# Optimization experiments

Measured on AMD Instinct MI355X. Metric: run time of the kernel, lower is better.

Reference implementation:

```python
import jax, jax.numpy as jnp
import numpy as np

HID = 10


def _lstm_cell(xt, h, c, W_ih, W_hh, b_ih, b_hh):
    # PyTorch LSTMCell: gates ordered (i, f, g, o)
    gates = xt @ W_ih.T + b_ih + h @ W_hh.T + b_hh  # [B, 4*HID]
    i, f, g, o = jnp.split(gates, 4, axis=-1)
    c_new = jax.nn.sigmoid(f) * c + jax.nn.sigmoid(i) * jnp.tanh(g)
    h_new = jax.nn.sigmoid(o) * jnp.tanh(c_new)
    return h_new, c_new


def setup_inputs() -> dict:
    key = jax.random.key(0)
    ks = jax.random.split(key, 12)
    B, T = 2048, 1024
    s = 0.1
    return {
        "x": jax.random.normal(ks[0], (B, T), dtype=jnp.float32),
        "W_ih1": jax.random.normal(ks[1], (4 * HID, 1), dtype=jnp.float32) * s,
        "W_hh1": jax.random.normal(ks[2], (4 * HID, HID), dtype=jnp.float32) * s,
        "b_ih1": jax.random.normal(ks[3], (4 * HID,), dtype=jnp.float32) * s,
        "b_hh1": jax.random.normal(ks[4], (4 * HID,), dtype=jnp.float32) * s,
        "W_ih2": jax.random.normal(ks[5], (4 * HID, HID), dtype=jnp.float32) * s,
        "W_hh2": jax.random.normal(ks[6], (4 * HID, HID), dtype=jnp.float32) * s,
        "b_ih2": jax.random.normal(ks[7], (4 * HID,), dtype=jnp.float32) * s,
        "b_ih2b": None,  # placeholder removed below
        "b_hh2": jax.random.normal(ks[8], (4 * HID,), dtype=jnp.float32) * s,
        "W_lin": jax.random.normal(ks[9], (1, HID), dtype=jnp.float32) * s,
        "b_lin": jax.random.normal(ks[10], (1,), dtype=jnp.float32) * s,
        "future": 64,
    } if False else {
        "x": jax.random.normal(ks[0], (B, T), dtype=jnp.float32),
        "W_ih1": jax.random.normal(ks[1], (4 * HID, 1), dtype=jnp.float32) * s,
        "W_hh1": jax.random.normal(ks[2], (4 * HID, HID), dtype=jnp.float32) * s,
        "b_ih1": jax.random.normal(ks[3], (4 * HID,), dtype=jnp.float32) * s,
        "b_hh1": jax.random.normal(ks[4], (4 * HID,), dtype=jnp.float32) * s,
        "W_ih2": jax.random.normal(ks[5], (4 * HID, HID), dtype=jnp.float32) * s,
        "W_hh2": jax.random.normal(ks[6], (4 * HID, HID), dtype=jnp.float32) * s,
        "b_ih2": jax.random.normal(ks[7], (4 * HID,), dtype=jnp.float32) * s,
        "b_hh2": jax.random.normal(ks[8], (4 * HID,), dtype=jnp.float32) * s,
        "W_lin": jax.random.normal(ks[9], (1, HID), dtype=jnp.float32) * s,
        "b_lin": jax.random.normal(ks[10], (1,), dtype=jnp.float32) * s,
        "future": 64,
    }


def _forward(x, W_ih1, W_hh1, b_ih1, b_hh1, W_ih2, W_hh2, b_ih2, b_hh2,
             W_lin, b_lin, future):
    B = x.shape[0]
    z = jnp.zeros((B, HID), dtype=x.dtype)
    state0 = (z, z, z, z)  # h1, c1, h2, c2

    def step(state, xt):
        h1, c1, h2, c2 = state
        h1, c1 = _lstm_cell(xt, h1, c1, W_ih1, W_hh1, b_ih1, b_hh1)
        h2, c2 = _lstm_cell(h1, h2, c2, W_ih2, W_hh2, b_ih2, b_hh2)
        y = h2 @ W_lin.T + b_lin  # [B, 1]
        return (h1, c1, h2, c2), y

    xs = x.T[:, :, None]  # [T, B, 1]
    state, ys = jax.lax.scan(step, state0, xs)  # ys: [T, B, 1]
    outs = ys[:, :, 0].T  # [B, T]

    if future > 0:
        last = ys[-1]  # [B, 1]

        def fstep(carry, _):
            state, y = carry
            state, y_new = step(state, y)
            return (state, y_new), y_new

        (_, _), fys = jax.lax.scan(fstep, (state, last), None, length=future)
        outs = jnp.concatenate([outs, fys[:, :, 0].T], axis=1)
    return outs  # [B, T + future]


def reference(x, W_ih1, W_hh1, b_ih1, b_hh1, W_ih2, W_hh2, b_ih2, b_hh2,
              W_lin, b_lin, future):
    return _forward(x, W_ih1, W_hh1, b_ih1, b_hh1, W_ih2, W_hh2, b_ih2,
                    b_hh2, W_lin, b_lin, future)
```

## Files before the change

kernel.cpp:

```cpp
#include <hip/hip_runtime.h>


#define NB 512
#define TMAIN 1024
#define HID 10
#define KCH 16
#define NCH (TMAIN / KCH)

typedef float v2f __attribute__((ext_vector_type(2)));
typedef float v4f __attribute__((ext_vector_type(4)));

#define PIN2(v) asm volatile("" : "+v"(v))
#define PIN(v)  asm volatile("" : "+v"(v))

__device__ __forceinline__ float rcp_(float v)  { return __builtin_amdgcn_rcpf(v); }
__device__ __forceinline__ float exp2_(float v) { return __builtin_amdgcn_exp2f(v); }
__device__ __forceinline__ v2f mk2(float x, float y) { v2f r; r.x = x; r.y = y; return r; }
__device__ __forceinline__ v2f pfma2(v2f a, v2f b, v2f c) { return __builtin_elementwise_fma(a, b, c); }

template<int J>
__device__ __forceinline__ float bc16(float v) {
    return __int_as_float(__builtin_amdgcn_ds_swizzle(__float_as_int(v), (J << 5) | 0x10));
}
__device__ __forceinline__ void bcast10(float h, float* hb) {
    hb[0] = bc16<0>(h); hb[1] = bc16<1>(h); hb[2] = bc16<2>(h); hb[3] = bc16<3>(h);
    hb[4] = bc16<4>(h); hb[5] = bc16<5>(h); hb[6] = bc16<6>(h); hb[7] = bc16<7>(h);
    hb[8] = bc16<8>(h); hb[9] = bc16<9>(h);
}

__global__ __launch_bounds__(128)
void lstm2_kernel(
    const float* __restrict__ x,
    const float* __restrict__ Wih1, const float* __restrict__ Whh1,
    const float* __restrict__ bih1, const float* __restrict__ bhh1,
    const float* __restrict__ Wih2, const float* __restrict__ Whh2,
    const float* __restrict__ bih2, const float* __restrict__ bhh2,
    const float* __restrict__ Wlin, const float* __restrict__ blin,
    const int* __restrict__ futp,
    float* __restrict__ out)
{
    const int tid  = threadIdx.x;
    const int wid  = tid >> 6;
    const int lane = tid & 63;
    const int e    = lane >> 4;
    const int u    = lane & 15;
    const int ge   = blockIdx.x * 4 + e;
    const int F    = futp[0];
    const int OUTW = TMAIN + F;

    __shared__ v4f   ringU[2][KCH][64];
    __shared__ float stC[64], stH[64];

    const bool uok = (u < HID);
    const int  uu  = uok ? u : 0;
    const int  Ri  = 0 * HID + uu;
    const int  Rf  = 1 * HID + uu;
    const int  Rg  = 2 * HID + uu;
    const int  Ro  = 3 * HID + uu;

    const float tK = 2.8853900817779268f;
    const float sK = -1.4426950408889634f;
    const float mu = uok ? 1.f : 0.f;
    const float sKm = mu * sK;
    const float tKm = mu * tK;

    v2f w1_if[10], w1_go[10], w2i_if[10], w2i_go[10], w2h_if[10], w2h_go[10];
    v2f wlp[5];
    #pragma unroll
    for (int j = 0; j < HID; ++j) {
        w1_if[j]  = mk2(sKm * Whh1[Ri*HID + j], sKm * Whh1[Rf*HID + j]);
        w1_go[j]  = mk2(tKm * Whh1[Rg*HID + j], sKm * Whh1[Ro*HID + j]);
        w2i_if[j] = mk2(sKm * Wih2[Ri*HID + j], sKm * Wih2[Rf*HID + j]);
        w2i_go[j] = mk2(tKm * Wih2[Rg*HID + j], sKm * Wih2[Ro*HID + j]);
        w2h_if[j] = mk2(sKm * Whh2[Ri*HID + j], sKm * Whh2[Rf*HID + j]);
        w2h_go[j] = mk2(tKm * Whh2[Rg*HID + j], sKm * Whh2[Ro*HID + j]);
    }
    #pragma unroll
    for (int k = 0; k < 5; ++k) wlp[k] = mk2(Wlin[2*k], Wlin[2*k + 1]);
    v2f b1_if = mk2(sKm * (bih1[Ri] + bhh1[Ri]), sKm * (bih1[Rf] + bhh1[Rf]));
    v2f b1_go = mk2(tKm * (bih1[Rg] + bhh1[Rg]), sKm * (bih1[Ro] + bhh1[Ro]));
    v2f b2_if = mk2(sKm * (bih2[Ri] + bhh2[Ri]), sKm * (bih2[Rf] + bhh2[Rf]));
    v2f b2_go = mk2(tKm * (bih2[Rg] + bhh2[Rg]), sKm * (bih2[Ro] + bhh2[Ro]));
    v2f wx_if = mk2(sKm * Wih1[Ri], sKm * Wih1[Rf]);
    v2f wx_go = mk2(tKm * Wih1[Rg], sKm * Wih1[Ro]);
    float bl = blin[0];

    #pragma unroll
    for (int j = 0; j < HID; ++j) {
        PIN2(w1_if[j]); PIN2(w1_go[j]); PIN2(w2i_if[j]); PIN2(w2i_go[j]);
        PIN2(w2h_if[j]); PIN2(w2h_go[j]);
    }
    #pragma unroll
    for (int k = 0; k < 5; ++k) PIN2(wlp[k]);
    PIN2(b1_if); PIN2(b1_go); PIN2(b2_if); PIN2(b2_go); PIN2(wx_if); PIN2(wx_go); PIN(bl);

    auto ctanh_ = [&](float cs) -> float {
        return fmaf(-2.0f, rcp_(1.0f + exp2_(cs)), 1.0f);
    };
    auto cellup2 = [&](v2f p_if, v2f p_go, float& c) -> float {
        v2f q_if, q_go;
        q_if.x = rcp_(1.0f + exp2_(p_if.x));
        q_if.y = rcp_(1.0f + exp2_(p_if.y));
        q_go.x = rcp_(1.0f + exp2_(p_go.x));
        q_go.y = rcp_(1.0f + exp2_(p_go.y));
        float g = fmaf(-2.0f * tK, q_go.x, tK);
        c = fmaf(q_if.y, c, q_if.x * g);
        return q_go.y * ctanh_(c);
    };
    auto dotp = [&](const v2f* w, const float* hb, v2f init) -> v2f {
        v2f P = pfma2(w[0], mk2(hb[0], hb[0]), init);
        v2f Q = w[1] * mk2(hb[1], hb[1]);
        #pragma unroll
        for (int j = 2; j < HID; j += 2) {
            P = pfma2(w[j],     mk2(hb[j],     hb[j]),     P);
            Q = pfma2(w[j + 1], mk2(hb[j + 1], hb[j + 1]), Q);
        }
        return P + Q;
    };

    float c1 = 0.f, c2 = 0.f, h1last = 0.f;
    float h1b[10], h2b[10];
    #pragma unroll
    for (int j = 0; j < HID; ++j) { h1b[j] = 0.f; h2b[j] = 0.f; }

    auto head_ = [&]() -> float {
        v2f Y = pfma2(wlp[0], mk2(h2b[0], h2b[1]), mk2(bl, 0.f));
        #pragma unroll
        for (int k = 1; k < 5; ++k)
            Y = pfma2(wlp[k], mk2(h2b[2*k], h2b[2*k + 1]), Y);
        return Y.x + Y.y;
    };

    auto pstep = [&](float xt, v4f* slot) {
        v2f A_if = dotp(w1_if, h1b, pfma2(wx_if, mk2(xt, xt), b1_if));
        v2f A_go = dotp(w1_go, h1b, pfma2(wx_go, mk2(xt, xt), b1_go));
        float h1n = cellup2(A_if, A_go, c1);
        h1last = h1n;
        bcast10(h1n, h1b);
        v2f U_if = dotp(w2i_if, h1b, b2_if);
        v2f U_go = dotp(w2i_go, h1b, b2_go);
        v4f U; U.x = U_if.x; U.y = U_if.y; U.z = U_go.x; U.w = U_go.y;
        slot[lane] = U;
    };
    auto cstep = [&](v4f U) -> float {
        v2f V_if = dotp(w2h_if, h2b, mk2(U.x, U.y));
        v2f V_go = dotp(w2h_go, h2b, mk2(U.z, U.w));
        float h2n = cellup2(V_if, V_go, c2);
        bcast10(h2n, h2b);
        return head_();
    };
    auto fstep = [&](float yt) -> float {
        v2f A_if = dotp(w1_if, h1b, pfma2(wx_if, mk2(yt, yt), b1_if));
        v2f A_go = dotp(w1_go, h1b, pfma2(wx_go, mk2(yt, yt), b1_go));
        float h1n = cellup2(A_if, A_go, c1);
        bcast10(h1n, h1b);
        v2f U_if = dotp(w2i_if, h1b, b2_if);
        v2f U_go = dotp(w2i_go, h1b, b2_go);
        v4f U; U.x = U_if.x; U.y = U_if.y; U.z = U_go.x; U.w = U_go.y;
        return cstep(U);
    };

    const float4* xrow = (const float4*)(x + (size_t)ge * TMAIN);
    float4* orow = (float4*)(out + (size_t)ge * OUTW);

    float4 xq0 = make_float4(0.f, 0.f, 0.f, 0.f);
    float4 xq1 = xq0, xq2 = xq0, xq3 = xq0;
    if (wid == 0) { xq0 = xrow[0]; xq1 = xrow[1]; xq2 = xrow[2]; xq3 = xrow[3]; }

    float yprev = 0.f;

    #pragma unroll 1
    for (int c = 0; c <= NCH; ++c) {
        if (wid == 0) {
            if (c < NCH) {
                float4 xn0 = make_float4(0.f, 0.f, 0.f, 0.f);
                float4 xn1 = xn0, xn2 = xn0, xn3 = xn0;
                if (c + 1 < NCH) {
                    xn0 = xrow[(c+1)*4+0]; xn1 = xrow[(c+1)*4+1];
                    xn2 = xrow[(c+1)*4+2]; xn3 = xrow[(c+1)*4+3];
                }
                v4f* rb = &ringU[c & 1][0][0];
                pstep(xq0.x, rb + 0*64);  pstep(xq0.y, rb + 1*64);
                pstep(xq0.z, rb + 2*64);  pstep(xq0.w, rb + 3*64);
                pstep(xq1.x, rb + 4*64);  pstep(xq1.y, rb + 5*64);
                pstep(xq1.z, rb + 6*64);  pstep(xq1.w, rb + 7*64);
                pstep(xq2.x, rb + 8*64);  pstep(xq2.y, rb + 9*64);
                pstep(xq2.z, rb + 10*64); pstep(xq2.w, rb + 11*64);
                pstep(xq3.x, rb + 12*64); pstep(xq3.y, rb + 13*64);
                pstep(xq3.z, rb + 14*64); pstep(xq3.w, rb + 15*64);
                if (c == NCH - 1) { stC[lane] = c1; stH[lane] = h1last; }
                xq0 = xn0; xq1 = xn1; xq2 = xn2; xq3 = xn3;
            }
        } else {
            if (c >= 1) {
                const v4f* rb = &ringU[(c - 1) & 1][0][0];
                #pragma unroll
                for (int q = 0; q < 4; ++q) {
                    v4f U0 = rb[(q*4 + 0)*64 + lane];
                    v4f U1 = rb[(q*4 + 1)*64 + lane];
                    v4f U2 = rb[(q*4 + 2)*64 + lane];
                    v4f U3 = rb[(q*4 + 3)*64 + lane];
                    float y0 = cstep(U0);
                    float y1 = cstep(U1);
                    float y2 = cstep(U2);
                    float y3 = cstep(U3);
                    if (u == 0) orow[(c - 1)*4 + q] = make_float4(y0, y1, y2, y3);
                    yprev = y3;
                }
            }
        }
        __syncthreads();
    }

    if (wid == 1) {
        c1 = stC[lane];
        bcast10(stH[lane], h1b);
        float yp = yprev;
        int t = 0;
        #pragma unroll 1
        for (; t + 3 < F; t += 4) {
            float y0 = fstep(yp);
            float y1 = fstep(y0);
            float y2 = fstep(y1);
            float y3 = fstep(y2);
            if (u == 0) orow[(TMAIN + t) / 4] = make_float4(y0, y1, y2, y3);
            yp = y3;
        }
        #pragma unroll 1
        for (; t < F; ++t) {
            yp = fstep(yp);
            if (u == 0) out[(size_t)ge * OUTW + TMAIN + t] = yp;
        }
    }
}

extern "C" void kernel_launch(void* const* d_in, const int* in_sizes, int n_in,
                              void* d_out, int out_size, void* d_ws, size_t ws_size,
                              hipStream_t stream) {
    const float* x    = (const float*)d_in[0];
    const float* Wih1 = (const float*)d_in[1];
    const float* Whh1 = (const float*)d_in[2];
    const float* bih1 = (const float*)d_in[3];
    const float* bhh1 = (const float*)d_in[4];
    const float* Wih2 = (const float*)d_in[5];
    const float* Whh2 = (const float*)d_in[6];
    const float* bih2 = (const float*)d_in[7];
    const float* bhh2 = (const float*)d_in[8];
    const float* Wlin = (const float*)d_in[9];
    const float* blin = (const float*)d_in[10];
    const int*   futp = (const int*)d_in[11];
    float* out = (float*)d_out;

    lstm2_kernel<<<NB, 128, 0, stream>>>(x, Wih1, Whh1, bih1, bhh1,
                                         Wih2, Whh2, bih2, bhh2,
                                         Wlin, blin, futp, out);
}
```

Before: 331.7 us.

## Split LSTM recurrence into four-wave pipeline with shared-memory rings

Extends the two-wave producer/consumer pipeline to four waves per block. Wave 0 runs only the layer-1 recurrence, wave 1 computes the non-recurrent layer-2 input projection from h1, wave 2 runs the layer-2 recurrence, and wave 3 computes the linear head and later the future steps. Each stage is offset by one chunk through double-buffered LDS rings. This shortens the serial critical path per wave so more recurrence work overlaps, at the cost of doubling threads per block, extra LDS traffic and two more pipeline fill chunks.

```diff
diff --git a/kernel.cpp b/kernel.cpp
--- a/kernel.cpp
+++ b/kernel.cpp
@@ -28,7 +28,7 @@
     hb[8] = bc16<8>(h); hb[9] = bc16<9>(h);
 }
 
-__global__ __launch_bounds__(128)
+__global__ __launch_bounds__(256)
 void lstm2_kernel(
     const float* __restrict__ x,
     const float* __restrict__ Wih1, const float* __restrict__ Whh1,
@@ -48,8 +48,10 @@
     const int F    = futp[0];
     const int OUTW = TMAIN + F;
 
-    __shared__ v4f   ringU[2][KCH][64];
-    __shared__ float stC[64], stH[64];
+    __shared__ __align__(16) float ringH1[2][KCH][64];
+    __shared__ __align__(16) v4f   ringU [2][KCH][64];
+    __shared__ __align__(16) float ringH2[2][KCH][64];
+    __shared__ __align__(16) float stC1[64], stH1[64], stC2[64], stH2[64];
 
     const bool uok = (u < HID);
     const int  uu  = uok ? u : 0;
@@ -117,8 +119,16 @@
         }
         return P + Q;
     };
-
-    float c1 = 0.f, c2 = 0.f, h1last = 0.f;
+    auto loadhb = [&](const float* base, float* hb) {
+        v4f a = *(const v4f*)(base);
+        v4f b = *(const v4f*)(base + 4);
+        v2f c = *(const v2f*)(base + 8);
+        hb[0] = a.x; hb[1] = a.y; hb[2] = a.z; hb[3] = a.w;
+        hb[4] = b.x; hb[5] = b.y; hb[6] = b.z; hb[7] = b.w;
+        hb[8] = c.x; hb[9] = c.y;
+    };
+
+    float c1 = 0.f, c2 = 0.f, h1last = 0.f, h2last = 0.f, yprev = 0.f;
     float h1b[10], h2b[10];
     #pragma unroll
     for (int j = 0; j < HID; ++j) { h1b[j] = 0.f; h2b[j] = 0.f; }
@@ -131,23 +141,13 @@
         return Y.x + Y.y;
     };
 
-    auto pstep = [&](float xt, v4f* slot) {
+    auto pstep0 = [&](float xt, float* hslot) -> float {
         v2f A_if = dotp(w1_if, h1b, pfma2(wx_if, mk2(xt, xt), b1_if));
         v2f A_go = dotp(w1_go, h1b, pfma2(wx_go, mk2(xt, xt), b1_go));
         float h1n = cellup2(A_if, A_go, c1);
-        h1last = h1n;
         bcast10(h1n, h1b);
-        v2f U_if = dotp(w2i_if, h1b, b2_if);
-        v2f U_go = dotp(w2i_go, h1b, b2_go);
-        v4f U; U.x = U_if.x; U.y = U_if.y; U.z = U_go.x; U.w = U_go.y;
-        slot[lane] = U;
-    };
-    auto cstep = [&](v4f U) -> float {
-        v2f V_if = dotp(w2h_if, h2b, mk2(U.x, U.y));
-        v2f V_go = dotp(w2h_go, h2b, mk2(U.z, U.w));
-        float h2n = cellup2(V_if, V_go, c2);
-        bcast10(h2n, h2b);
-        return head_();
+        hslot[lane] = h1n;
+        return h1n;
     };
     auto fstep = [&](float yt) -> float {
         v2f A_if = dotp(w1_if, h1b, pfma2(wx_if, mk2(yt, yt), b1_if));
@@ -156,55 +156,85 @@
         bcast10(h1n, h1b);
         v2f U_if = dotp(w2i_if, h1b, b2_if);
         v2f U_go = dotp(w2i_go, h1b, b2_go);
-        v4f U; U.x = U_if.x; U.y = U_if.y; U.z = U_go.x; U.w = U_go.y;
-        return cstep(U);
+        v2f V_if = dotp(w2h_if, h2b, mk2(U_if.x, U_if.y));
+        v2f V_go = dotp(w2h_go, h2b, mk2(U_go.x, U_go.y));
+        float h2n = cellup2(V_if, V_go, c2);
+        bcast10(h2n, h2b);
+        return head_();
     };
 
     const float4* xrow = (const float4*)(x + (size_t)ge * TMAIN);
     float4* orow = (float4*)(out + (size_t)ge * OUTW);
 
-    float4 xq0 = make_float4(0.f, 0.f, 0.f, 0.f);
-    float4 xq1 = xq0, xq2 = xq0, xq3 = xq0;
+    float4 z4 = make_float4(0.f, 0.f, 0.f, 0.f);
+    float4 xq0 = z4, xq1 = z4, xq2 = z4, xq3 = z4;
     if (wid == 0) { xq0 = xrow[0]; xq1 = xrow[1]; xq2 = xrow[2]; xq3 = xrow[3]; }
 
-    float yprev = 0.f;
-
     #pragma unroll 1
-    for (int c = 0; c <= NCH; ++c) {
+    for (int c = 0; c <= NCH + 2; ++c) {
         if (wid == 0) {
             if (c < NCH) {
-                float4 xn0 = make_float4(0.f, 0.f, 0.f, 0.f);
-                float4 xn1 = xn0, xn2 = xn0, xn3 = xn0;
+                float4 xn0 = z4, xn1 = z4, xn2 = z4, xn3 = z4;
                 if (c + 1 < NCH) {
                     xn0 = xrow[(c+1)*4+0]; xn1 = xrow[(c+1)*4+1];
                     xn2 = xrow[(c+1)*4+2]; xn3 = xrow[(c+1)*4+3];
                 }
-                v4f* rb = &ringU[c & 1][0][0];
-                pstep(xq0.x, rb + 0*64);  pstep(xq0.y, rb + 1*64);
-                pstep(xq0.z, rb + 2*64);  pstep(xq0.w, rb + 3*64);
-                pstep(xq1.x, rb + 4*64);  pstep(xq1.y, rb + 5*64);
-                pstep(xq1.z, rb + 6*64);  pstep(xq1.w, rb + 7*64);
-                pstep(xq2.x, rb + 8*64);  pstep(xq2.y, rb + 9*64);
-                pstep(xq2.z, rb + 10*64); pstep(xq2.w, rb + 11*64);
-                pstep(xq3.x, rb + 12*64); pstep(xq3.y, rb + 13*64);
-                pstep(xq3.z, rb + 14*64); pstep(xq3.w, rb + 15*64);
-                if (c == NCH - 1) { stC[lane] = c1; stH[lane] = h1last; }
+                float* hs = &ringH1[c & 1][0][0];
+                h1last = pstep0(xq0.x, hs + 0*64);  h1last = pstep0(xq0.y, hs + 1*64);
+                h1last = pstep0(xq0.z, hs + 2*64);  h1last = pstep0(xq0.w, hs + 3*64);
+                h1last = pstep0(xq1.x, hs + 4*64);  h1last = pstep0(xq1.y, hs + 5*64);
+                h1last = pstep0(xq1.z, hs + 6*64);  h1last = pstep0(xq1.w, hs + 7*64);
+                h1last = pstep0(xq2.x, hs + 8*64);  h1last = pstep0(xq2.y, hs + 9*64);
+                h1last = pstep0(xq2.z, hs + 10*64); h1last = pstep0(xq2.w, hs + 11*64);
+                h1last = pstep0(xq3.x, hs + 12*64); h1last = pstep0(xq3.y, hs + 13*64);
+                h1last = pstep0(xq3.z, hs + 14*64); h1last = pstep0(xq3.w, hs + 15*64);
+                if (c == NCH - 1) { stC1[lane] = c1; stH1[lane] = h1last; }
                 xq0 = xn0; xq1 = xn1; xq2 = xn2; xq3 = xn3;
             }
+        } else if (wid == 1) {
+            const int cc = c - 1;
+            if (cc >= 0 && cc < NCH) {
+                const float* hs = &ringH1[cc & 1][0][0];
+                v4f* us = &ringU[cc & 1][0][0];
+                #pragma unroll
+                for (int t = 0; t < KCH; ++t) {
+                    float hb[10];
+                    loadhb(hs + t*64 + e*16, hb);
+                    v2f U_if = dotp(w2i_if, hb, b2_if);
+                    v2f U_go = dotp(w2i_go, hb, b2_go);
+                    v4f U; U.x = U_if.x; U.y = U_if.y; U.z = U_go.x; U.w = U_go.y;
+                    us[t*64 + lane] = U;
+                }
+            }
+        } else if (wid == 2) {
+            const int cc = c - 2;
+            if (cc >= 0 && cc < NCH) {
+                const v4f* us = &ringU[cc & 1][0][0];
+                float* h2s = &ringH2[cc & 1][0][0];
+                #pragma unroll
+                for (int t = 0; t < KCH; ++t) {
+                    v4f U = us[t*64 + lane];
+                    v2f V_if = dotp(w2h_if, h2b, mk2(U.x, U.y));
+                    v2f V_go = dotp(w2h_go, h2b, mk2(U.z, U.w));
+                    float h2n = cellup2(V_if, V_go, c2);
+                    bcast10(h2n, h2b);
+                    h2s[t*64 + lane] = h2n;
+                    h2last = h2n;
+                }
+                if (cc == NCH - 1) { stC2[lane] = c2; stH2[lane] = h2last; }
+            }
         } else {
-            if (c >= 1) {
-                const v4f* rb = &ringU[(c - 1) & 1][0][0];
+            const int cc = c - 3;
+            if (cc >= 0 && cc < NCH) {
+                const float* h2s = &ringH2[cc & 1][0][0];
                 #pragma unroll
                 for (int q = 0; q < 4; ++q) {
-                    v4f U0 = rb[(q*4 + 0)*64 + lane];
-                    v4f U1 = rb[(q*4 + 1)*64 + lane];
-                    v4f U2 = rb[(q*4 + 2)*64 + lane];
-                    v4f U3 = rb[(q*4 + 3)*64 + lane];
-                    float y0 = cstep(U0);
-                    float y1 = cstep(U1);
-                    float y2 = cstep(U2);
-                    float y3 = cstep(U3);
-                    if (u == 0) orow[(c - 1)*4 + q] = make_float4(y0, y1, y2, y3);
+                    float y0, y1, y2, y3;
+                    loadhb(h2s + (q*4 + 0)*64 + e*16, h2b); y0 = head_();
+                    loadhb(h2s + (q*4 + 1)*64 + e*16, h2b); y1 = head_();
+                    loadhb(h2s + (q*4 + 2)*64 + e*16, h2b); y2 = head_();
+                    loadhb(h2s + (q*4 + 3)*64 + e*16, h2b); y3 = head_();
+                    if (u == 0) orow[cc*4 + q] = make_float4(y0, y1, y2, y3);
                     yprev = y3;
                 }
             }
@@ -212,9 +242,11 @@
         __syncthreads();
     }
 
-    if (wid == 1) {
-        c1 = stC[lane];
-        bcast10(stH[lane], h1b);
+    if (wid == 3) {
+        c1 = stC1[lane];
+        c2 = stC2[lane];
+        loadhb(&stH1[e*16], h1b);
+        loadhb(&stH2[e*16], h2b);
         float yp = yprev;
         int t = 0;
         #pragma unroll 1
@@ -251,7 +283,7 @@
     const int*   futp = (const int*)d_in[11];
     float* out = (float*)d_out;
 
-    lstm2_kernel<<<NB, 128, 0, stream>>>(x, Wih1, Whh1, bih1, bhh1,
+    lstm2_kernel<<<NB, 256, 0, stream>>>(x, Wih1, Whh1, bih1, bhh1,
                                          Wih2, Whh2, bih2, bhh2,
                                          Wlin, blin, futp, out);
 }
```

Result: faster. 324.2 us (-2.3%).
